# Performance work log

Hardware: AMD Instinct MI355X
Metric: run time of the kernel (lower is better)

Reference implementation:

```python
import jax, jax.numpy as jnp
from jax import lax
import numpy as np

B, T, D, H, DH, FF, K = 16, 1024, 512, 8, 64, 2048, 3
EPS = 1e-5


def _layer_norm(x, g, b):
    mu = jnp.mean(x, axis=-1, keepdims=True)
    var = jnp.mean((x - mu) ** 2, axis=-1, keepdims=True)
    return (x - mu) / jnp.sqrt(var + EPS) * g + b


def setup_inputs() -> dict:
    key = jax.random.key(0)
    ks = jax.random.split(key, 14)
    f32 = jnp.float32
    dec_inp = jax.random.normal(ks[0], (B, T, D), f32)
    lengths = jax.random.randint(ks[1], (B,), T // 2, T + 1)
    mask = (jnp.arange(T)[None, :] < lengths[:, None])[:, :, None]  # [B,T,1] bool
    qkv_w = jax.random.normal(ks[2], (3 * H * DH, D), f32) * (D ** -0.5)
    qkv_b = jnp.zeros((3 * H * DH,), f32)
    o_w = jax.random.normal(ks[3], (D, H * DH), f32) * ((H * DH) ** -0.5)
    ln1_g = jnp.ones((D,), f32)
    ln1_b = jnp.zeros((D,), f32)
    conv1_w = jax.random.normal(ks[4], (FF, D, K), f32) * ((D * K) ** -0.5)
    conv1_b = jnp.zeros((FF,), f32)
    conv2_w = jax.random.normal(ks[5], (D, FF, K), f32) * ((FF * K) ** -0.5)
    conv2_b = jnp.zeros((D,), f32)
    ln2_g = jnp.ones((D,), f32)
    ln2_b = jnp.zeros((D,), f32)
    return dict(dec_inp=dec_inp, mask=mask, qkv_w=qkv_w, qkv_b=qkv_b, o_w=o_w,
                ln1_g=ln1_g, ln1_b=ln1_b, conv1_w=conv1_w, conv1_b=conv1_b,
                conv2_w=conv2_w, conv2_b=conv2_b, ln2_g=ln2_g, ln2_b=ln2_b)


def reference(dec_inp, mask, qkv_w, qkv_b, o_w, ln1_g, ln1_b,
              conv1_w, conv1_b, conv2_w, conv2_b, ln2_g, ln2_b):
    # ----- MultiHeadAttn (post-norm, dropout = identity in eval) -----
    attn_mask = ~mask[:, :, 0]                      # [B,T], True = pad
    qkv = dec_inp @ qkv_w.T + qkv_b                 # [B,T,3*H*DH]
    q, k, v = jnp.split(qkv, 3, axis=2)

    def to_heads(x):  # [B,T,H*DH] -> [B*H,T,DH] (batch-major, as in torch)
        return x.reshape(B, T, H, DH).transpose(0, 2, 1, 3).reshape(B * H, T, DH)

    q, k, v = to_heads(q), to_heads(k), to_heads(v)
    scores = jnp.einsum('bqd,bkd->bqk', q, k) * (DH ** -0.5)  # [B*H,T,T]
    # faithful to torch: mask tiled head-major (index i % B)
    am = jnp.tile(attn_mask[:, None, :], (H, T, 1))           # [B*H,T,T]
    scores = jnp.where(am, -jnp.inf, scores)
    prob = jax.nn.softmax(scores, axis=2)
    vec = jnp.einsum('bqk,bkd->bqd', prob, v)                 # [B*H,T,DH]
    # faithful to torch: view as [H,B,...] then permute
    vec = vec.reshape(H, B, T, DH).transpose(1, 2, 0, 3).reshape(B, T, H * DH)
    attn_out = vec @ o_w.T                                    # [B,T,D]
    out = _layer_norm(dec_inp + attn_out, ln1_g, ln1_b)
    out = out * mask

    # ----- PositionwiseConvFF (post-norm) -----
    x = out.transpose(0, 2, 1)                                # [B,D,T]
    h = lax.conv_general_dilated(x, conv1_w, (1,), [(K // 2, K // 2)],
                                 dimension_numbers=('NCH', 'OIH', 'NCH'))
    h = jax.nn.relu(h + conv1_b[None, :, None])
    h = lax.conv_general_dilated(h, conv2_w, (1,), [(K // 2, K // 2)],
                                 dimension_numbers=('NCH', 'OIH', 'NCH'))
    core = (h + conv2_b[None, :, None]).transpose(0, 2, 1)    # [B,T,D]
    out = _layer_norm(out + core, ln2_g, ln2_b)
    return out * mask
```

## Files before the change

kernel.cpp:

```cpp
#include <hip/hip_runtime.h>

using h16 = _Float16;
using h16x4 = __attribute__((ext_vector_type(4))) _Float16;
using h16x8 = __attribute__((ext_vector_type(8))) _Float16;
using f32x4 = __attribute__((ext_vector_type(4))) float;

static constexpr int cB = 16, cT = 1024, cD = 512, cH = 8, cDH = 64, cFF = 2048;
static constexpr int cM = cB * cT;
static constexpr int cTP = cT + 2;

__device__ __forceinline__ bool mask_val(const void* mb, int idx) {
  const unsigned char* u8 = (const unsigned char*)mb;
  if (u8[1] == 1) return u8[idx] != 0;
  const float* f = (const float*)mb;
  if (f[1] == 1.0f) return f[idx] != 0.0f;
  return ((const int*)mb)[idx] != 0;
}

__device__ __forceinline__ void gl_lds16(const h16* g, h16* l) {
  __builtin_amdgcn_global_load_lds(
      (const __attribute__((address_space(1))) unsigned int*)g,
      (__attribute__((address_space(3))) unsigned int*)l, 16, 0, 0);
}


__global__ __launch_bounds__(256) void k_cast4(const float* __restrict__ in,
                                               h16* __restrict__ out, int n4) {
  int i = blockIdx.x * 256 + threadIdx.x;
  if (i >= n4) return;
  const float4 f = ((const float4*)in)[i];
  h16x4 o = {(h16)f.x, (h16)f.y, (h16)f.z, (h16)f.w};
  ((h16x4*)out)[i] = o;
}

__global__ __launch_bounds__(256) void k_repack_w1(const float* __restrict__ w,
                                                   h16* __restrict__ out) {
  int i = blockIdx.x * 256 + threadIdx.x;
  if (i >= cFF * cD) return;
  int f = i >> 9, d = i & 511;
#pragma unroll
  for (int k = 0; k < 3; ++k)
    out[f * (3 * cD) + k * cD + d] = (h16)w[(long)i * 3 + k];
}

__global__ __launch_bounds__(256) void k_repack_w2(const float* __restrict__ w,
                                                   h16* __restrict__ out) {
  int i = blockIdx.x * 256 + threadIdx.x;
  if (i >= cD * cFF) return;
  int o = i >> 11, f = i & 2047;
#pragma unroll
  for (int k = 0; k < 3; ++k)
    out[o * (3 * cFF) + k * cFF + f] = (h16)w[(long)i * 3 + k];
}

__global__ __launch_bounds__(256) void k_zero_pads(h16* __restrict__ xp,
                                                   h16* __restrict__ hp) {
  int i = blockIdx.x * 256 + threadIdx.x;
  if (i < cB * 2 * cD) {
    int b = i / (2 * cD); int rr = (i / cD) & 1; int c = i % cD;
    xp[((long)b * cTP + rr * (cTP - 1)) * cD + c] = (h16)0.f;
  }
  if (i < cB * 2 * cFF) {
    int b = i / (2 * cFF); int rr = (i / cFF) & 1; int c = i % cFF;
    hp[((long)b * cTP + rr * (cTP - 1)) * cFF + c] = (h16)0.f;
  }
}

template <int SKIP, bool A_CONV, bool OUT_CONV, bool BIAS, bool RELU,
          bool OUT_H16, bool VSCAT, int SPLITK, bool SWIZ>
__global__ __launch_bounds__(256)
void gemm_bt(const h16* __restrict__ A, const h16* __restrict__ W,
             const float* __restrict__ bias, void* __restrict__ Cv,
             h16* __restrict__ Vg, const void* __restrict__ maskbuf,
             int ldc, int Kd, int lda, long zstride) {
  __shared__ h16 smem[2 * 128 * 64];
  h16* As = smem;
  h16* Bs = smem + 128 * 64;
  const int tid = threadIdx.x;
  const int w = tid >> 6, l = tid & 63;
  int m0, n0;
  if (SWIZ) {
    m0 = (blockIdx.x * 16 + (blockIdx.y >> 2)) * 128;
    n0 = (blockIdx.y & 3) * 128;
  } else {
    m0 = blockIdx.y * 128;
    n0 = blockIdx.x * 128;
  }

  if (SKIP == 1) {
    if (!mask_val(maskbuf, m0)) return;
  } else if (SKIP == 2) {
    int t0 = m0 & 1023, base = ((m0 >> 10) & 1) * 8;
    bool need = false;
#pragma unroll
    for (int i = 0; i < 8; ++i) need |= mask_val(maskbuf, ((base + i) << 10) + t0);
    if (!need) return;
  } else if (SKIP == 3) {
    int t0 = m0 & 1023;
    if (t0 && !mask_val(maskbuf, m0 - 1)) return;
  }

  const int wm = (w >> 1) * 64, wn = (w & 1) * 64;
  const int lr = l >> 3;
  const int lcs = ((l & 7) ^ lr) * 8;
  const int fr = l & 15;
  const int fb = fr & 7;
  const int qd = l >> 4;

  const int kspan = (SPLITK == 2) ? (Kd >> 1) : Kd;
  const int kbeg = (SPLITK == 2) ? blockIdx.z * kspan : 0;
  const int kend = kbeg + kspan;

  f32x4 zero4 = {0.f, 0.f, 0.f, 0.f};
  f32x4 acc[4][4];
#pragma unroll
  for (int mi = 0; mi < 4; ++mi)
#pragma unroll
    for (int ni = 0; ni < 4; ++ni) acc[mi][ni] = zero4;

  for (int k0 = kbeg; k0 < kend; k0 += 64) {
    __syncthreads();
#pragma unroll
    for (int i = 0; i < 4; ++i) {
      int c = w * 4 + i;
      int ar = m0 + c * 8 + lr;
      long aoff = (long)(ar + (A_CONV ? 2 * (ar >> 10) : 0)) * lda + k0 + lcs;
      gl_lds16(A + aoff, &As[c * 512]);
      int br = n0 + c * 8 + lr;
      long boff = (long)br * Kd + k0 + lcs;
      gl_lds16(W + boff, &Bs[c * 512]);
    }
    __syncthreads();
#pragma unroll
    for (int kc = 0; kc < 2; ++kc) {
      h16x8 af[4], bfr[4];
#pragma unroll
      for (int mi = 0; mi < 4; ++mi)
        af[mi] = *(const h16x8*)&As[(wm + mi * 16 + fr) * 64 +
                                    (((kc * 4 + qd) ^ fb) * 8)];
#pragma unroll
      for (int ni = 0; ni < 4; ++ni)
        bfr[ni] = *(const h16x8*)&Bs[(wn + ni * 16 + fr) * 64 +
                                     (((kc * 4 + qd) ^ fb) * 8)];
#pragma unroll
      for (int mi = 0; mi < 4; ++mi)
#pragma unroll
        for (int ni = 0; ni < 4; ++ni)
          acc[mi][ni] = __builtin_amdgcn_mfma_f32_16x16x32_f16(
              af[mi], bfr[ni], acc[mi][ni], 0, 0, 0);
    }
  }
  const bool do_bias = BIAS && (SPLITK == 1 || blockIdx.z == 0);
  if (VSCAT && n0 >= 1024) {
#pragma unroll
    for (int mi = 0; mi < 4; ++mi) {
      int t0 = (m0 + wm + mi * 16 + (l >> 4) * 4) & 1023;
      int jj = ((m0 >> 10) << 3);
#pragma unroll
      for (int ni = 0; ni < 4; ++ni) {
        int gc = n0 + wn + ni * 16 + fr;
        int dh = gc & 63;
        int j2 = jj + ((gc - 1024) >> 6);
        float bb = do_bias ? bias[gc] : 0.f;
        h16x4 v4 = {(h16)(acc[mi][ni][0] + bb), (h16)(acc[mi][ni][1] + bb),
                    (h16)(acc[mi][ni][2] + bb), (h16)(acc[mi][ni][3] + bb)};
        *(h16x4*)&Vg[((long)j2 * 64 + dh) * 1024 + t0] = v4;
      }
    }
  } else if (OUT_H16) {
    __syncthreads();
#pragma unroll
    for (int mi = 0; mi < 4; ++mi) {
#pragma unroll
      for (int ni = 0; ni < 4; ++ni) {
#pragma unroll
        for (int rr = 0; rr < 4; ++rr) {
          int rrow = wm + mi * 16 + (l >> 4) * 4 + rr;
          int ccol = wn + ni * 16 + fr;
          float v = acc[mi][ni][rr];
          if (do_bias) v += bias[n0 + ccol];
          if (RELU) v = v > 0.f ? v : 0.f;
          smem[rrow * 128 + ccol] = (h16)v;
        }
      }
    }
    __syncthreads();
    h16* outp = (h16*)Cv + (SPLITK == 2 ? (long)blockIdx.z * zstride : 0);
    const int r2 = tid >> 4, c2 = (tid & 15) * 8;
#pragma unroll
    for (int i = 0; i < 8; ++i) {
      int row = r2 + i * 16;
      int gr = m0 + row;
      long orow = (long)gr + (OUT_CONV ? (2 * (gr >> 10) + 1) : 0);
      *(h16x8*)&outp[orow * ldc + n0 + c2] = *(h16x8*)&smem[row * 128 + c2];
    }
  } else {
#pragma unroll
    for (int mi = 0; mi < 4; ++mi) {
#pragma unroll
      for (int ni = 0; ni < 4; ++ni) {
#pragma unroll
        for (int rr = 0; rr < 4; ++rr) {
          int gr = m0 + wm + mi * 16 + (l >> 4) * 4 + rr;
          int gc = n0 + wn + ni * 16 + fr;
          float v = acc[mi][ni][rr];
          if (do_bias) v += bias[gc];
          if (RELU) v = v > 0.f ? v : 0.f;
          long orow = (long)gr + (OUT_CONV ? (2 * (gr >> 10) + 1) : 0);
          ((float*)Cv)[orow * ldc + gc] = v;
        }
      }
    }
  }
}

template <int SKIP, bool A_CONV, bool OUT_CONV, bool BIAS, bool RELU,
          int SPLITK, int NBLK_LOG2>
__global__ __launch_bounds__(1024, 4)
void gemm16(const h16* __restrict__ A, const h16* __restrict__ W,
            const float* __restrict__ bias, h16* __restrict__ C,
            const void* __restrict__ maskbuf, int ldc, int Kd, int lda,
            long zstride) {
  extern __shared__ h16 sm[];
  const int tid = threadIdx.x;
  const int wid = tid >> 6, l = tid & 63;
  const int m0 = (blockIdx.x * 8 + (blockIdx.y >> NBLK_LOG2)) * 256;
  const int n0 = (blockIdx.y & ((1 << NBLK_LOG2) - 1)) * 256;

  if (SKIP == 1) {
    if (!mask_val(maskbuf, m0)) return;
  } else if (SKIP == 3) {
    int t0 = m0 & 1023;
    if (t0 && !mask_val(maskbuf, m0 - 1)) return;
  }

  const int wm = wid >> 2, wn = wid & 3;
  const int fr = l & 15, qd = l >> 4, fb = fr & 7;
  const int lr = l >> 3;
  const int lcs = ((l & 7) ^ lr) * 8;

  const int kspan = (SPLITK == 2) ? (Kd >> 1) : Kd;
  const int kbeg = (SPLITK == 2) ? blockIdx.z * kspan : 0;
  const int nt = kspan >> 6;

  f32x4 zero4 = {0.f, 0.f, 0.f, 0.f};
  f32x4 acc[4][4];
#pragma unroll
  for (int m = 0; m < 4; ++m)
#pragma unroll
    for (int n = 0; n < 4; ++n) acc[m][n] = zero4;

  auto stage = [&](int ti) {
    h16* Ab = sm + (ti & 1) * 32768;
    h16* Bb = Ab + 16384;
#pragma unroll
    for (int i = 0; i < 2; ++i) {
      int c = wid * 2 + i;
      int ar = m0 + c * 8 + lr;
      long aoff = (long)(ar + (A_CONV ? 2 * (ar >> 10) : 0)) * lda +
                  kbeg + ti * 64 + lcs;
      gl_lds16(A + aoff, &Ab[c * 512]);
      int br = n0 + c * 8 + lr;
      long boff = (long)br * Kd + kbeg + ti * 64 + lcs;
      gl_lds16(W + boff, &Bb[c * 512]);
    }
  };

  const int arow = wm * 64 + fr;
  const int brow = wn * 64 + fr;
  const int sA = (qd ^ fb) * 8;
  const int sB = ((4 + qd) ^ fb) * 8;

  stage(0);
  if (nt > 1) stage(1);
  asm volatile("s_waitcnt vmcnt(4)" ::: "memory");
  __builtin_amdgcn_s_barrier();

  for (int t = 0; t < nt; ++t) {
    const h16* Ab = sm + (t & 1) * 32768;
    const h16* Bb = Ab + 16384;
    const bool pf = (t + 2 < nt);
    h16x8 a[4], b[4];
#pragma unroll
    for (int m = 0; m < 4; ++m)
      a[m] = *(const h16x8*)&Ab[(arow + m * 16) * 64 + sA];
#pragma unroll
    for (int n = 0; n < 4; ++n)
      b[n] = *(const h16x8*)&Bb[(brow + n * 16) * 64 + sA];
    __builtin_amdgcn_s_setprio(1);
#pragma unroll
    for (int m = 0; m < 4; ++m)
#pragma unroll
      for (int n = 0; n < 4; ++n)
        acc[m][n] = __builtin_amdgcn_mfma_f32_16x16x32_f16(a[m], b[n],
                                                           acc[m][n], 0, 0, 0);
    __builtin_amdgcn_s_setprio(0);
    h16x8 a2[4], b2[4];
#pragma unroll
    for (int m = 0; m < 4; ++m)
      a2[m] = *(const h16x8*)&Ab[(arow + m * 16) * 64 + sB];
#pragma unroll
    for (int n = 0; n < 4; ++n)
      b2[n] = *(const h16x8*)&Bb[(brow + n * 16) * 64 + sB];
    asm volatile("s_waitcnt lgkmcnt(0)" ::: "memory");
    __builtin_amdgcn_s_barrier();
    if (pf) stage(t + 2);
    __builtin_amdgcn_s_setprio(1);
#pragma unroll
    for (int m = 0; m < 4; ++m)
#pragma unroll
      for (int n = 0; n < 4; ++n)
        acc[m][n] = __builtin_amdgcn_mfma_f32_16x16x32_f16(a2[m], b2[n],
                                                           acc[m][n], 0, 0, 0);
    __builtin_amdgcn_s_setprio(0);
    if (pf)
      asm volatile("s_waitcnt vmcnt(4)" ::: "memory");
    else
      asm volatile("s_waitcnt vmcnt(0)" ::: "memory");
    __builtin_amdgcn_s_barrier();
  }

  const bool do_bias = BIAS && (SPLITK == 1 || blockIdx.z == 0);
  const int qd4 = qd * 4;
#pragma unroll
  for (int m = 0; m < 4; ++m) {
    int row = wm * 64 + m * 16 + qd4;
#pragma unroll
    for (int n = 0; n < 4; ++n) {
      int col = wn * 64 + n * 16 + fr;
      float bb = do_bias ? bias[n0 + col] : 0.f;
#pragma unroll
      for (int rr = 0; rr < 4; ++rr) {
        float v = acc[m][n][rr] + bb;
        if (RELU) v = v > 0.f ? v : 0.f;
        sm[(row + rr) * 256 + col] = (h16)v;
      }
    }
  }
  __syncthreads();
  h16* outp = C + (SPLITK == 2 ? (long)blockIdx.z * zstride : 0);
  const int r2 = tid >> 5, c2 = (tid & 31) * 8;
#pragma unroll
  for (int i = 0; i < 8; ++i) {
    int row = r2 + i * 32;
    int gr = m0 + row;
    long orow = (long)gr + (OUT_CONV ? (2 * (gr >> 10) + 1) : 0);
    *(h16x8*)&outp[orow * (long)ldc + n0 + c2] = *(h16x8*)&sm[row * 256 + c2];
  }
}

__global__ __launch_bounds__(256)
void k_attn(const h16* __restrict__ qk, const h16* __restrict__ Vg,
            const void* __restrict__ maskbuf, h16* __restrict__ attn_out) {
  __shared__ h16 Ks[64 * 64];
  __shared__ h16 Vt[64 * 64];
  __shared__ h16 Ps[4][16 * 68];
  __shared__ float sbias[64];
  const int tid = threadIdx.x, w = tid >> 6, l = tid & 63;
  const int f = blockIdx.x;
  const int bp = f & 15, qt = (f >> 4) & 15, hp = f >> 8;
  const int j = hp * 16 + bp;
  const int bd = j >> 3, hd = j & 7;

  if (!mask_val(maskbuf, bp * cT + qt * 64)) return;

  const int fr = l & 15, fq = (l >> 4) * 8;
  const int fb = fr & 7, qd = l >> 4;
  const int lr = l >> 3, lcs = ((l & 7) ^ lr) * 8;

  h16x8 qf[2];
#pragma unroll
  for (int kc = 0; kc < 2; ++kc) {
    qf[kc] = *(const h16x8*)&qk[
        (long)((bd << 10) + qt * 64 + w * 16 + fr) * 1024 +
        hd * 64 + kc * 32 + fq];
    qf[kc] *= (h16)0.125f;
  }

  f32x4 zero4 = {0.f, 0.f, 0.f, 0.f};
  f32x4 o[4];
  float lrow[4];
#pragma unroll
  for (int nt = 0; nt < 4; ++nt) o[nt] = zero4;
#pragma unroll
  for (int r = 0; r < 4; ++r) lrow[r] = 0.f;

  for (int k0 = 0; k0 < cT; k0 += 64) {
    if (!mask_val(maskbuf, bp * cT + k0)) break;
    __syncthreads();
#pragma unroll
    for (int i = 0; i < 2; ++i) {
      int c = w * 2 + i;
      int row = c * 8 + lr;
      gl_lds16(qk + (long)((bd << 10) + k0 + row) * 1024 + 512 + hd * 64 + lcs,
               &Ks[c * 512]);
      gl_lds16(Vg + ((long)j * 64 + row) * 1024 + k0 + lcs, &Vt[c * 512]);
    }
    if (tid < 64)
      sbias[tid] = mask_val(maskbuf, bp * cT + k0 + tid) ? 0.f : -1e30f;
    __syncthreads();

    f32x4 S[4];
#pragma unroll
    for (int kt = 0; kt < 4; ++kt) {
      float sb = sbias[kt * 16 + fr];
      f32x4 s = {sb, sb, sb, sb};
#pragma unroll
      for (int kc = 0; kc < 2; ++kc) {
        h16x8 kf = *(const h16x8*)&Ks[(kt * 16 + fr) * 64 +
                                      (((kc * 4 + qd) ^ fb) * 8)];
        s = __builtin_amdgcn_mfma_f32_16x16x32_f16(qf[kc], kf, s, 0, 0, 0);
      }
      S[kt] = s;
    }
#pragma unroll
    for (int r = 0; r < 4; ++r) {
      float p0 = __expf(S[0][r] - 4.f), p1 = __expf(S[1][r] - 4.f);
      float p2 = __expf(S[2][r] - 4.f), p3 = __expf(S[3][r] - 4.f);
      lrow[r] += (p0 + p1) + (p2 + p3);
      int ql = (l >> 4) * 4 + r;
      Ps[w][ql * 68 + fr] = (h16)p0;
      Ps[w][ql * 68 + 16 + fr] = (h16)p1;
      Ps[w][ql * 68 + 32 + fr] = (h16)p2;
      Ps[w][ql * 68 + 48 + fr] = (h16)p3;
    }
#pragma unroll
    for (int kp = 0; kp < 2; ++kp) {
      h16x8 pf = *(const h16x8*)&Ps[w][fr * 68 + kp * 32 + fq];
#pragma unroll
      for (int nt = 0; nt < 4; ++nt) {
        h16x8 vf = *(const h16x8*)&Vt[(nt * 16 + fr) * 64 +
                                      (((kp * 4 + qd) ^ fb) * 8)];
        o[nt] = __builtin_amdgcn_mfma_f32_16x16x32_f16(pf, vf, o[nt], 0, 0, 0);
      }
    }
  }
#pragma unroll
  for (int r = 0; r < 4; ++r) {
#pragma unroll
    for (int m = 1; m < 16; m <<= 1) lrow[r] += __shfl_xor(lrow[r], m);
    float inv = 1.f / lrow[r];
    int q = qt * 64 + w * 16 + (l >> 4) * 4 + r;
    long row = (long)bp * cT + q;
#pragma unroll
    for (int nt = 0; nt < 4; ++nt)
      attn_out[row * cD + hp * 64 + nt * 16 + fr] = (h16)(o[nt][r] * inv);
  }
}

template <bool WRITE_XP, bool RH16, bool R2H16>
__global__ __launch_bounds__(256)
void k_ln(const float* __restrict__ X, const void* __restrict__ Rv,
          const void* __restrict__ Rv2,
          const float* __restrict__ g, const float* __restrict__ bta,
          const void* __restrict__ maskbuf,
          float* __restrict__ outf, h16* __restrict__ xp) {
  const int w = threadIdx.x >> 6, l = threadIdx.x & 63;
  const long row = (long)blockIdx.x * 4 + w;
  const float4* x4 = (const float4*)(X + row * cD);
  float4 a0 = x4[l], a1 = x4[l + 64];
  float v[8];
  if (RH16) {
    const h16x4* r4 = (const h16x4*)((const h16*)Rv + row * cD);
    h16x4 b0 = r4[l], b1 = r4[l + 64];
    v[0] = a0.x + (float)b0[0]; v[1] = a0.y + (float)b0[1];
    v[2] = a0.z + (float)b0[2]; v[3] = a0.w + (float)b0[3];
    v[4] = a1.x + (float)b1[0]; v[5] = a1.y + (float)b1[1];
    v[6] = a1.z + (float)b1[2]; v[7] = a1.w + (float)b1[3];
  } else {
    const float4* r4 = (const float4*)((const float*)Rv + row * cD);
    float4 b0 = r4[l], b1 = r4[l + 64];
    v[0] = a0.x + b0.x; v[1] = a0.y + b0.y; v[2] = a0.z + b0.z; v[3] = a0.w + b0.w;
    v[4] = a1.x + b1.x; v[5] = a1.y + b1.y; v[6] = a1.z + b1.z; v[7] = a1.w + b1.w;
  }
  if (R2H16) {
    const h16x4* r4 = (const h16x4*)((const h16*)Rv2 + row * cD);
    h16x4 b0 = r4[l], b1 = r4[l + 64];
    v[0] += (float)b0[0]; v[1] += (float)b0[1];
    v[2] += (float)b0[2]; v[3] += (float)b0[3];
    v[4] += (float)b1[0]; v[5] += (float)b1[1];
    v[6] += (float)b1[2]; v[7] += (float)b1[3];
  }
  float s = 0.f;
#pragma unroll
  for (int i = 0; i < 8; ++i) s += v[i];
#pragma unroll
  for (int m = 1; m < 64; m <<= 1) s += __shfl_xor(s, m);
  const float mu = s * (1.f / 512.f);
  float s2 = 0.f;
#pragma unroll
  for (int i = 0; i < 8; ++i) { float d = v[i] - mu; s2 += d * d; }
#pragma unroll
  for (int m = 1; m < 64; m <<= 1) s2 += __shfl_xor(s2, m);
  const float rstd = rsqrtf(s2 * (1.f / 512.f) + 1e-5f);
  const float mv = mask_val(maskbuf, (int)row) ? 1.f : 0.f;
  const float4* g4 = (const float4*)g;
  const float4* t4 = (const float4*)bta;
  float4 g0 = g4[l], g1 = g4[l + 64], t0 = t4[l], t1 = t4[l + 64];
  float4 y0, y1;
  y0.x = ((v[0] - mu) * rstd * g0.x + t0.x) * mv;
  y0.y = ((v[1] - mu) * rstd * g0.y + t0.y) * mv;
  y0.z = ((v[2] - mu) * rstd * g0.z + t0.z) * mv;
  y0.w = ((v[3] - mu) * rstd * g0.w + t0.w) * mv;
  y1.x = ((v[4] - mu) * rstd * g1.x + t1.x) * mv;
  y1.y = ((v[5] - mu) * rstd * g1.y + t1.y) * mv;
  y1.z = ((v[6] - mu) * rstd * g1.z + t1.z) * mv;
  y1.w = ((v[7] - mu) * rstd * g1.w + t1.w) * mv;
  ((float4*)(outf + row * cD))[l] = y0;
  ((float4*)(outf + row * cD))[l + 64] = y1;
  if (WRITE_XP) {
    const long xrow = row + 2 * (row >> 10) + 1;
    h16x4 h0 = {(h16)y0.x, (h16)y0.y, (h16)y0.z, (h16)y0.w};
    h16x4 h1 = {(h16)y1.x, (h16)y1.y, (h16)y1.z, (h16)y1.w};
    ((h16x4*)(xp + xrow * cD))[l] = h0;
    ((h16x4*)(xp + xrow * cD))[l + 64] = h1;
  }
}

extern "C" void kernel_launch(void* const* d_in, const int* in_sizes, int n_in,
                              void* d_out, int out_size, void* d_ws, size_t ws_size,
                              hipStream_t stream) {
  const float* dec   = (const float*)d_in[0];
  const void*  maskb = d_in[1];
  const float* qkv_w = (const float*)d_in[2];
  const float* qkv_b = (const float*)d_in[3];
  const float* o_w   = (const float*)d_in[4];
  const float* ln1g  = (const float*)d_in[5];
  const float* ln1b  = (const float*)d_in[6];
  const float* c1w   = (const float*)d_in[7];
  const float* c1b   = (const float*)d_in[8];
  const float* c2w   = (const float*)d_in[9];
  const float* c2b   = (const float*)d_in[10];
  const float* ln2g  = (const float*)d_in[11];
  const float* ln2b  = (const float*)d_in[12];

  char* p = (char*)d_ws;
  auto alloc = [&](size_t bytes) {
    char* r = p; p += (bytes + 255) & ~(size_t)255; return r;
  };
  h16*   dec_h  = (h16*)alloc((size_t)cM * cD * 2);
  h16*   qkvw_h = (h16*)alloc((size_t)1536 * cD * 2);
  h16*   ow_h   = (h16*)alloc((size_t)cD * cD * 2);
  h16*   w1p    = (h16*)alloc((size_t)cFF * 3 * cD * 2);
  h16*   w2p    = (h16*)alloc((size_t)cD * 3 * cFF * 2);
  h16*   qk_h   = (h16*)alloc((size_t)cM * 1024 * 2);
  h16*   vg     = (h16*)alloc((size_t)cB * cH * cDH * cT * 2);
  h16*   attn_h = (h16*)alloc((size_t)cM * cD * 2);
  float* tmp    = (float*)alloc((size_t)cM * cD * 4);
  float* out1   = (float*)alloc((size_t)cM * cD * 4);
  h16*   xp     = (h16*)alloc((size_t)cB * cTP * cD * 2);
  h16*   hp     = (h16*)alloc((size_t)cB * cTP * cFF * 2);
  h16*   core0 = attn_h;
  h16*   core1 = qk_h;
  (void)ws_size; (void)n_in; (void)in_sizes; (void)out_size;

  static bool s_attr = false;
  if (!s_attr) {
    hipFuncSetAttribute(
        reinterpret_cast<const void*>(&gemm16<3, true, true, true, true, 1, 3>),
        hipFuncAttributeMaxDynamicSharedMemorySize, 131072);
    hipFuncSetAttribute(
        reinterpret_cast<const void*>(&gemm16<1, true, false, true, false, 2, 1>),
        hipFuncAttributeMaxDynamicSharedMemorySize, 131072);
    s_attr = true;
  }

  k_cast4<<<(cM * cD / 4 + 255) / 256, 256, 0, stream>>>(dec, dec_h, cM * cD / 4);
  k_cast4<<<(1536 * cD / 4 + 255) / 256, 256, 0, stream>>>(qkv_w, qkvw_h, 1536 * cD / 4);
  k_cast4<<<(cD * cD / 4 + 255) / 256, 256, 0, stream>>>(o_w, ow_h, cD * cD / 4);
  k_repack_w1<<<(cFF * cD + 255) / 256, 256, 0, stream>>>(c1w, w1p);
  k_repack_w2<<<(cD * cFF + 255) / 256, 256, 0, stream>>>(c2w, w2p);
  k_zero_pads<<<(cB * 2 * cFF + 255) / 256, 256, 0, stream>>>(xp, hp);

  gemm_bt<2, false, false, true, false, true, true, 1, false>
      <<<dim3(12, cM / 128), 256, 0, stream>>>(dec_h, qkvw_h, qkv_b, qk_h, vg,
                                               maskb, 1024, cD, cD, 0);

  k_attn<<<dim3(2048), 256, 0, stream>>>(qk_h, vg, maskb, attn_h);

  gemm_bt<1, false, false, false, false, false, false, 1, false>
      <<<dim3(cD / 128, cM / 128), 256, 0, stream>>>(attn_h, ow_h, nullptr, tmp,
                                                     nullptr, maskb, cD, cD, cD, 0);

  k_ln<true, false, false><<<cM / 4, 256, 0, stream>>>(dec, tmp, nullptr, ln1g,
                                                       ln1b, maskb, out1, xp);

  gemm16<3, true, true, true, true, 1, 3>
      <<<dim3(8, 64), dim3(1024), 131072, stream>>>(xp, w1p, c1b, hp, maskb,
                                                    cFF, 3 * cD, cD, 0);

  gemm16<1, true, false, true, false, 2, 1>
      <<<dim3(8, 16, 2), dim3(1024), 131072, stream>>>(hp, w2p, c2b, core0,
                                                       maskb, cD, 3 * cFF, cFF,
                                                       (long)(core1 - core0));

  k_ln<false, true, true><<<cM / 4, 256, 0, stream>>>(out1, core0, core1, ln2g,
                                                      ln2b, maskb,
                                                      (float*)d_out, nullptr);
}
```

Baseline: 487.7 us.

## Switch GEMM to 4-stage K=32 pipeline with k-chunk-major LDS layout

The GEMM main loop now processes K in 32-wide slices with a four-buffer LDS ring and prefetches three slices ahead instead of two 64-wide double-buffered slices. The LDS tile is stored k-chunk-major (row index within each 8-element chunk) so fragment reads are contiguous without the XOR swizzle, and one barrier per iteration replaces two. This aims to hide global-load latency better and cut per-iteration synchronization, at the cost of twice as many loop iterations and barriers per K, and possible LDS bank conflicts from the new layout. The LDS footprint stays 64K halves.

```diff
diff --git a/kernel.cpp b/kernel.cpp
--- a/kernel.cpp
+++ b/kernel.cpp
@@ -235,13 +235,11 @@
   }
 
   const int wm = wid >> 2, wn = wid & 3;
-  const int fr = l & 15, qd = l >> 4, fb = fr & 7;
-  const int lr = l >> 3;
-  const int lcs = ((l & 7) ^ lr) * 8;
+  const int fr = l & 15, qd = l >> 4;
 
   const int kspan = (SPLITK == 2) ? (Kd >> 1) : Kd;
   const int kbeg = (SPLITK == 2) ? blockIdx.z * kspan : 0;
-  const int nt = kspan >> 6;
+  const int nt = kspan >> 5;
 
   f32x4 zero4 = {0.f, 0.f, 0.f, 0.f};
   f32x4 acc[4][4];
@@ -250,43 +248,37 @@
 #pragma unroll
     for (int n = 0; n < 4; ++n) acc[m][n] = zero4;
 
+  const int srow = tid & 255, sch = tid >> 8;
+  const int ar0 = m0 + srow;
+  const long arow_off =
+      (long)(ar0 + (A_CONV ? 2 * (ar0 >> 10) : 0)) * lda + kbeg + sch * 8;
+  const long brow_off = (long)(n0 + srow) * Kd + kbeg + sch * 8;
   auto stage = [&](int ti) {
-    h16* Ab = sm + (ti & 1) * 32768;
-    h16* Bb = Ab + 16384;
-#pragma unroll
-    for (int i = 0; i < 2; ++i) {
-      int c = wid * 2 + i;
-      int ar = m0 + c * 8 + lr;
-      long aoff = (long)(ar + (A_CONV ? 2 * (ar >> 10) : 0)) * lda +
-                  kbeg + ti * 64 + lcs;
-      gl_lds16(A + aoff, &Ab[c * 512]);
-      int br = n0 + c * 8 + lr;
-      long boff = (long)br * Kd + kbeg + ti * 64 + lcs;
-      gl_lds16(W + boff, &Bb[c * 512]);
-    }
+    h16* Ab = sm + (ti & 3) * 16384;
+    gl_lds16(A + arow_off + ti * 32, &Ab[wid * 512]);
+    gl_lds16(W + brow_off + ti * 32, &Ab[8192 + wid * 512]);
   };
 
-  const int arow = wm * 64 + fr;
-  const int brow = wn * 64 + fr;
-  const int sA = (qd ^ fb) * 8;
-  const int sB = ((4 + qd) ^ fb) * 8;
+  const int abase = (qd * 256 + wm * 64 + fr) * 8;
+  const int bbase = (qd * 256 + wn * 64 + fr) * 8;
 
   stage(0);
   if (nt > 1) stage(1);
+  if (nt > 2) stage(2);
   asm volatile("s_waitcnt vmcnt(4)" ::: "memory");
   __builtin_amdgcn_s_barrier();
 
   for (int t = 0; t < nt; ++t) {
-    const h16* Ab = sm + (t & 1) * 32768;
-    const h16* Bb = Ab + 16384;
-    const bool pf = (t + 2 < nt);
+    const h16* Ab = sm + (t & 3) * 16384;
+    const h16* Bb = Ab + 8192;
     h16x8 a[4], b[4];
 #pragma unroll
     for (int m = 0; m < 4; ++m)
-      a[m] = *(const h16x8*)&Ab[(arow + m * 16) * 64 + sA];
+      a[m] = *(const h16x8*)&Ab[abase + m * 128];
 #pragma unroll
     for (int n = 0; n < 4; ++n)
-      b[n] = *(const h16x8*)&Bb[(brow + n * 16) * 64 + sA];
+      b[n] = *(const h16x8*)&Bb[bbase + n * 128];
+    if (t + 3 < nt) stage(t + 3);
     __builtin_amdgcn_s_setprio(1);
 #pragma unroll
     for (int m = 0; m < 4; ++m)
@@ -295,26 +287,10 @@
         acc[m][n] = __builtin_amdgcn_mfma_f32_16x16x32_f16(a[m], b[n],
                                                            acc[m][n], 0, 0, 0);
     __builtin_amdgcn_s_setprio(0);
-    h16x8 a2[4], b2[4];
-#pragma unroll
-    for (int m = 0; m < 4; ++m)
-      a2[m] = *(const h16x8*)&Ab[(arow + m * 16) * 64 + sB];
-#pragma unroll
-    for (int n = 0; n < 4; ++n)
-      b2[n] = *(const h16x8*)&Bb[(brow + n * 16) * 64 + sB];
-    asm volatile("s_waitcnt lgkmcnt(0)" ::: "memory");
-    __builtin_amdgcn_s_barrier();
-    if (pf) stage(t + 2);
-    __builtin_amdgcn_s_setprio(1);
-#pragma unroll
-    for (int m = 0; m < 4; ++m)
-#pragma unroll
-      for (int n = 0; n < 4; ++n)
-        acc[m][n] = __builtin_amdgcn_mfma_f32_16x16x32_f16(a2[m], b2[n],
-                                                           acc[m][n], 0, 0, 0);
-    __builtin_amdgcn_s_setprio(0);
-    if (pf)
+    if (t + 3 < nt)
       asm volatile("s_waitcnt vmcnt(4)" ::: "memory");
+    else if (t + 2 < nt)
+      asm volatile("s_waitcnt vmcnt(2)" ::: "memory");
     else
       asm volatile("s_waitcnt vmcnt(0)" ::: "memory");
     __builtin_amdgcn_s_barrier();
```

After: 749.5 us. 53.7% more time.
